# Performance work log

Hardware: AMD Instinct MI355X
Metric: run time of the kernel (lower is better)

The kernel has to match this reference:

```python
import jax, jax.numpy as jnp
import numpy as np
import math

DIM, DIM_QK, DIM_V = 1024, 128, 1024
NUM_BUCKETS, MAX_DISTANCE = 32, 128


def silu(x):
    return x * jax.nn.sigmoid(x)


def laplacian_attn_fn(x):
    mu = math.sqrt(0.5)
    std = math.sqrt(0.25 * math.pi)
    return (1.0 + jax.lax.erf((x - mu) / (std * math.sqrt(2.0)))) * 0.5


def rel_pos_bias(seq_len, table, scale):
    # causal T5 bucketing: n = q_pos - k_pos, clamped at 0
    q_pos = jnp.arange(seq_len)
    k_pos = jnp.arange(seq_len)
    rel_pos = k_pos[None, :] - q_pos[:, None]  # [i, j]
    n = jnp.maximum(-rel_pos, 0)
    max_exact = NUM_BUCKETS // 2
    is_small = n < max_exact
    n_safe = jnp.maximum(n, 1).astype(jnp.float32)
    val_if_large = max_exact + (
        jnp.log(n_safe / max_exact) / math.log(MAX_DISTANCE / max_exact)
        * (NUM_BUCKETS - max_exact)
    ).astype(jnp.int32)
    val_if_large = jnp.minimum(val_if_large, NUM_BUCKETS - 1)
    bucket = jnp.where(is_small, n, val_if_large)
    return table[bucket] * scale  # [i, j]


def setup_inputs() -> dict:
    key = jax.random.key(0)
    ks = jax.random.split(key, 8)
    B, S = 4, 2048
    lin_std_qk = 1.0 / math.sqrt(DIM)
    return {
        "x": jax.random.normal(ks[0], (B, S, DIM), dtype=jnp.float32),
        "wqk": jax.random.uniform(ks[1], (DIM, DIM_QK), minval=-lin_std_qk, maxval=lin_std_qk, dtype=jnp.float32),
        "bqk": jnp.zeros((DIM_QK,), dtype=jnp.float32),
        "gamma": 1.0 + 0.02 * jax.random.normal(ks[2], (2, DIM_QK), dtype=jnp.float32),
        "beta": jnp.zeros((2, DIM_QK), dtype=jnp.float32),
        "wv": jax.random.uniform(ks[3], (DIM, DIM_V), minval=-lin_std_qk, maxval=lin_std_qk, dtype=jnp.float32),
        "bv": jnp.zeros((DIM_V,), dtype=jnp.float32),
        "rel_bias": jax.random.normal(ks[4], (NUM_BUCKETS,), dtype=jnp.float32),
    }


def reference(x, wqk, bqk, gamma, beta, wv, bv, rel_bias):
    B, S, _ = x.shape
    qk = silu(x @ wqk + bqk)                       # [B, S, dqk]
    q = qk * gamma[0] + beta[0]
    k = qk * gamma[1] + beta[1]
    v = silu(x @ wv + bv)                          # [B, S, dv]
    scale = 1.0 / S                                # laplacian_attn_fn scaling
    sim = jnp.einsum('bid,bjd->bij', q, k) * scale
    sim = sim + rel_pos_bias(S, rel_bias, DIM_QK ** 0.5)[None, :, :]
    attn = laplacian_attn_fn(sim)
    causal_mask = jnp.triu(jnp.ones((S, S), dtype=bool), k=1)
    attn = jnp.where(causal_mask[None, :, :], 0.0, attn)
    return jnp.einsum('bij,bjd->bid', attn, v)
```

## Files before the change

### kernel.cpp

```cpp
#include <hip/hip_runtime.h>
#include <stdint.h>


#define B_   4
#define S_   2048
#define DIM_ 1024
#define DQK  128
#define DV   1024
#define NQV  1152

typedef __attribute__((ext_vector_type(8))) short short8;
typedef __attribute__((ext_vector_type(4))) float f32x4;

__device__ __forceinline__ uint16_t f32_to_bf16(float f) {
  uint32_t u = __float_as_uint(f);
  u += 0x7FFFu + ((u >> 16) & 1u);
  return (uint16_t)(u >> 16);
}

__device__ __forceinline__ uint32_t pack_bf16(float a, float b) {
  return (uint32_t)f32_to_bf16(a) | ((uint32_t)f32_to_bf16(b) << 16);
}

__device__ __forceinline__ float silu_f(float x) {
  return x * __builtin_amdgcn_rcpf(1.0f + __expf(-x));
}

__device__ __forceinline__ float laplacian_attn(float x) {
  float z  = (x - 0.70710678118654752f) * 0.79788456080286536f;
  float az = fabsf(z);
  float t  = __builtin_amdgcn_rcpf(fmaf(0.3275911f, az, 1.0f));
  float w  = fmaf(1.061405429f, t, -1.453152027f);
  w = fmaf(w, t, 1.421413741f);
  w = fmaf(w, t, -0.284496736f);
  w = fmaf(w, t, 0.254829592f);
  float P  = w * t;
  float E  = __expf(-z * z);
  float ea = fmaf(-P, E, 1.0f);
  float er = copysignf(ea, z);
  return fmaf(0.5f, er, 0.5f);
}

__device__ __forceinline__ void gload16(const uint16_t* g, uint16_t* l) {
  __builtin_amdgcn_global_load_lds(
      (const __attribute__((address_space(1))) void*)g,
      (__attribute__((address_space(3))) void*)l, 16, 0, 0);
}

template <int MT, int NT, int DEPTH>
__device__ __forceinline__ void wave_gemm_t(
    const uint16_t* __restrict__ A, int KBa, int rbA,
    const uint16_t* __restrict__ Bt, int KBb, int rbB,
    int nkb, f32x4 acc[MT][NT])
{
  const int lane = threadIdx.x & 63;

  const uint16_t* pa[MT];
  const uint16_t* pb[NT];
  #pragma unroll
  for (int mt = 0; mt < MT; mt++)
    pa[mt] = A + (size_t)(rbA + mt) * KBa * 512 + lane * 8;
  #pragma unroll
  for (int nt = 0; nt < NT; nt++)
    pb[nt] = Bt + (size_t)(rbB + nt) * KBb * 512 + lane * 8;

  #pragma unroll
  for (int mt = 0; mt < MT; mt++)
    #pragma unroll
    for (int nt = 0; nt < NT; nt++) {
      f32x4 z = {0.0f, 0.0f, 0.0f, 0.0f};
      acc[mt][nt] = z;
    }

  short8 fa0[MT], fb0[NT], fa1[MT], fb1[NT];

  auto loads = [&](short8 fa[MT], short8 fb[NT], int kb) {
    #pragma unroll
    for (int mt = 0; mt < MT; mt++)
      fa[mt] = *(const short8*)(pa[mt] + (size_t)kb * 512);
    #pragma unroll
    for (int nt = 0; nt < NT; nt++)
      fb[nt] = *(const short8*)(pb[nt] + (size_t)kb * 512);
  };
  auto mfmas = [&](short8 fa[MT], short8 fb[NT]) {
    #pragma unroll
    for (int mt = 0; mt < MT; mt++)
      #pragma unroll
      for (int nt = 0; nt < NT; nt++)
        acc[mt][nt] = __builtin_amdgcn_mfma_f32_16x16x32_bf16(
            fa[mt], fb[nt], acc[mt][nt], 0, 0, 0);
  };

  if constexpr (DEPTH == 2) {
    loads(fa0, fb0, 0);
    loads(fa1, fb1, 1);
    for (int kb = 2; kb < nkb; kb += 2) {
      mfmas(fa0, fb0);
      loads(fa0, fb0, kb);
      mfmas(fa1, fb1);
      loads(fa1, fb1, kb + 1);
    }
    mfmas(fa0, fb0);
    mfmas(fa1, fb1);
  } else {
    short8 fa2[MT], fb2[NT], fa3[MT], fb3[NT];
    loads(fa0, fb0, 0);
    loads(fa1, fb1, 1);
    loads(fa2, fb2, 2);
    loads(fa3, fb3, 3);
    for (int kb = 4; kb < nkb; kb += 4) {
      mfmas(fa0, fb0);
      loads(fa0, fb0, kb);
      mfmas(fa1, fb1);
      loads(fa1, fb1, kb + 1);
      mfmas(fa2, fb2);
      loads(fa2, fb2, kb + 2);
      mfmas(fa3, fb3);
      loads(fa3, fb3, kb + 3);
    }
    mfmas(fa0, fb0);
    mfmas(fa1, fb1);
    mfmas(fa2, fb2);
    mfmas(fa3, fb3);
  }
}

__global__ __launch_bounds__(256) void k_prep(
    const float* __restrict__ x, const float* __restrict__ wqk,
    const float* __restrict__ wv, const float* __restrict__ rel,
    uint16_t* __restrict__ xb, uint16_t* __restrict__ wT,
    float* __restrict__ bias_n)
{
  int blk = blockIdx.x;
  if (blk < 4096) {
    int t = blk * 256 + threadIdx.x;
    int i16 = t & 15, oct = (t >> 4) & 3, kb = (t >> 6) & 31, ib = t >> 11;
    const float* src = x + (size_t)(ib * 16 + i16) * DIM_ + kb * 32 + oct * 8;
    float4 a = *(const float4*)src;
    float4 b = *(const float4*)(src + 4);
    short8 o;
    o[0] = f32_to_bf16(a.x); o[1] = f32_to_bf16(a.y);
    o[2] = f32_to_bf16(a.z); o[3] = f32_to_bf16(a.w);
    o[4] = f32_to_bf16(b.x); o[5] = f32_to_bf16(b.y);
    o[6] = f32_to_bf16(b.z); o[7] = f32_to_bf16(b.w);
    *(short8*)(xb + (size_t)t * 8) = o;
  } else if (blk < 4672) {
    int t = (blk - 4096) * 256 + threadIdx.x;
    int n16 = t & 15, oct = (t >> 4) & 3, kb = (t >> 6) & 31, nb = t >> 11;
    int n = nb * 16 + n16;
    int k0 = kb * 32 + oct * 8;
    short8 o;
    if (n < DQK) {
      #pragma unroll
      for (int j = 0; j < 8; j++)
        o[j] = f32_to_bf16(wqk[(size_t)(k0 + j) * DQK + n]);
    } else {
      int nn = n - DQK;
      #pragma unroll
      for (int j = 0; j < 8; j++)
        o[j] = f32_to_bf16(wv[(size_t)(k0 + j) * DV + nn]);
    }
    *(short8*)(wT + (size_t)t * 8) = o;
  } else {
    for (int n = threadIdx.x; n < S_; n += 256) {
      int bucket;
      if (n < 16) {
        bucket = n;
      } else {
        float tt = logf((float)n * 0.0625f) / 2.0794415416798357f * 16.0f;
        int vl = 16 + (int)tt;
        bucket = vl < 31 ? vl : 31;
      }
      bias_n[n] = rel[bucket] * 11.313708498984761f;
    }
  }
}


__global__ __launch_bounds__(256, 4) void k_gemm_qkv(
    const uint16_t* __restrict__ xb, const uint16_t* __restrict__ wT,
    const float* __restrict__ bqk, const float* __restrict__ gamma,
    const float* __restrict__ beta, const float* __restrict__ bv,
    uint16_t* __restrict__ qb, uint16_t* __restrict__ kb,
    uint16_t* __restrict__ vT)
{
  int L = blockIdx.x;
  int c = L & 7;
  int idx = L >> 3;
  int by = c + 8 * (idx / 9);
  int bx = idx % 9;
  int lane = threadIdx.x & 63;
  int wave = threadIdx.x >> 6;
  int lane16 = lane & 15;
  int quad = lane >> 4;
  int wrow = (wave >> 1) * 64;
  int wcol = (wave & 1) * 64;

  __shared__ uint16_t sA[8 * 2 * 512];
  __shared__ uint16_t sB[8 * 2 * 512];

  const uint16_t *Ab, *Bb;
  if (bx == 0) { Ab = wT;                              Bb = xb + (size_t)by * 8 * 32 * 512; }
  else         { Ab = xb + (size_t)by * 8 * 32 * 512;  Bb = wT + (size_t)bx * 8 * 32 * 512; }

  const uint16_t* gp = (wave >> 1) ? Bb : Ab;
  uint16_t*       sp = (wave >> 1) ? sB : sA;
  int rb0 = (wave & 1) * 4;

  f32x4 acc[4][4];
  #pragma unroll
  for (int mt = 0; mt < 4; mt++)
    #pragma unroll
    for (int nt = 0; nt < 4; nt++) {
      f32x4 z = {0.0f, 0.0f, 0.0f, 0.0f};
      acc[mt][nt] = z;
    }

  for (int kbi = 0; kbi < 32; kbi += 2) {
    #pragma unroll
    for (int uu = 0; uu < 8; uu++) {
      int rbu = rb0 + (uu >> 1), kk = uu & 1;
      gload16(gp + ((size_t)rbu * 32 + kbi + kk) * 512 + lane * 8,
              sp + (rbu * 2 + kk) * 512);
    }
    __syncthreads();
    #pragma unroll
    for (int kk = 0; kk < 2; kk++) {
      short8 fa[4], fb[4];
      #pragma unroll
      for (int mt = 0; mt < 4; mt++)
        fa[mt] = *(const short8*)(sA + (((wave >> 1) * 4 + mt) * 2 + kk) * 512 + lane * 8);
      #pragma unroll
      for (int nt = 0; nt < 4; nt++)
        fb[nt] = *(const short8*)(sB + (((wave & 1) * 4 + nt) * 2 + kk) * 512 + lane * 8);
      #pragma unroll
      for (int mt = 0; mt < 4; mt++)
        #pragma unroll
        for (int nt = 0; nt < 4; nt++)
          acc[mt][nt] = __builtin_amdgcn_mfma_f32_16x16x32_bf16(
              fa[mt], fb[nt], acc[mt][nt], 0, 0, 0);
    }
    __syncthreads();
  }

  if (bx == 0) {
    int ibase = by * 128 + (wave & 1) * 64;
    int cbase = (wave >> 1) * 64;
    #pragma unroll
    for (int mt = 0; mt < 4; mt++) {
      int c0 = cbase + mt * 16 + quad * 4;
      float4 bb = *(const float4*)(bqk + c0);
      float4 g0 = *(const float4*)(gamma + c0);
      float4 g1 = *(const float4*)(gamma + DQK + c0);
      float4 e0 = *(const float4*)(beta + c0);
      float4 e1 = *(const float4*)(beta + DQK + c0);
      size_t coff = (size_t)(c0 >> 5) * 512 + ((c0 >> 3) & 3) * 128 + (c0 & 7);
      #pragma unroll
      for (int nt = 0; nt < 4; nt++) {
        int i = ibase + nt * 16 + lane16;
        float s0 = silu_f(acc[mt][nt][0] + bb.x);
        float s1 = silu_f(acc[mt][nt][1] + bb.y);
        float s2 = silu_f(acc[mt][nt][2] + bb.z);
        float s3 = silu_f(acc[mt][nt][3] + bb.w);
        uint2 pq, pk;
        pq.x = pack_bf16(fmaf(s0, g0.x, e0.x), fmaf(s1, g0.y, e0.y));
        pq.y = pack_bf16(fmaf(s2, g0.z, e0.z), fmaf(s3, g0.w, e0.w));
        pk.x = pack_bf16(fmaf(s0, g1.x, e1.x), fmaf(s1, g1.y, e1.y));
        pk.y = pack_bf16(fmaf(s2, g1.z, e1.z), fmaf(s3, g1.w, e1.w));
        size_t off = (size_t)(i >> 4) * 4 * 512 + (size_t)(i & 15) * 8 + coff;
        *(uint2*)(qb + off) = pq;
        *(uint2*)(kb + off) = pk;
      }
    }
  } else {
    int b = by >> 4;
    uint16_t* vt = vT + (size_t)b * DV * S_;
    #pragma unroll
    for (int nt = 0; nt < 4; nt++) {
      int n = (bx - 1) * 128 + wcol + nt * 16 + lane16;
      float bb = bv[n];
      #pragma unroll
      for (int mt = 0; mt < 4; mt++) {
        int j0l = (by & 15) * 128 + wrow + mt * 16 + quad * 4;
        uint16_t v0 = f32_to_bf16(silu_f(acc[mt][nt][0] + bb));
        uint16_t v1 = f32_to_bf16(silu_f(acc[mt][nt][1] + bb));
        uint16_t v2 = f32_to_bf16(silu_f(acc[mt][nt][2] + bb));
        uint16_t v3 = f32_to_bf16(silu_f(acc[mt][nt][3] + bb));
        size_t off = (size_t)((n >> 4) * 64 + (j0l >> 5)) * 512 +
                     ((j0l >> 3) & 3) * 128 + (n & 15) * 8 + (j0l & 7);
        uint2 pk;
        pk.x = (uint32_t)v0 | ((uint32_t)v1 << 16);
        pk.y = (uint32_t)v2 | ((uint32_t)v3 << 16);
        *(uint2*)(vt + off) = pk;
      }
    }
  }
}

__global__ __launch_bounds__(128, 6) void k_gemm_sim(
    const uint16_t* __restrict__ qb, const uint16_t* __restrict__ kb,
    const float* __restrict__ bias_n, uint16_t* __restrict__ attn)
{
  int b = blockIdx.x;
  int bt = blockIdx.y;
  int it = (int)((sqrtf(8.0f * (float)b + 1.0f) - 1.0f) * 0.5f);
  while ((it + 1) * (it + 2) / 2 <= b) ++it;
  while (it * (it + 1) / 2 > b) --it;
  int jt = b - it * (it + 1) / 2;

  int lane = threadIdx.x & 63;
  int wave = threadIdx.x >> 6;
  int lane16 = lane & 15;
  int quad = lane >> 4;

  f32x4 acc[4][2];
  wave_gemm_t<4,2,4>(kb, 4, bt * 128 + jt * 4,
                     qb, 4, bt * 128 + it * 4 + wave * 2,
                     4, acc);

  uint16_t* ab = attn + (size_t)bt * S_ * S_;
  int ibase = it * 64 + wave * 32;
  int jbase = jt * 64;
  #pragma unroll
  for (int nt = 0; nt < 2; nt++) {
    int i = ibase + nt * 16 + lane16;
    size_t irow = (size_t)(i >> 4) * 64 * 512 + (size_t)(i & 15) * 8;
    #pragma unroll
    for (int mt = 0; mt < 4; mt++) {
      int j0 = jbase + mt * 16 + quad * 4;
      float v[4];
      #pragma unroll
      for (int r = 0; r < 4; r++) {
        int j = j0 + r;
        float aval = 0.0f;
        if (j <= i) {
          float sim = acc[mt][nt][r] * (1.0f / 2048.0f) + bias_n[i - j];
          aval = laplacian_attn(sim);
        }
        v[r] = aval;
      }
      uint2 pk;
      pk.x = pack_bf16(v[0], v[1]);
      pk.y = pack_bf16(v[2], v[3]);
      size_t off = irow + (size_t)(j0 >> 5) * 512 + ((j0 >> 3) & 3) * 128 +
                   (j0 & 7);
      *(uint2*)(ab + off) = pk;
    }
  }
}

__global__ __launch_bounds__(256, 4) void k_gemm_out(
    const uint16_t* __restrict__ attn, const uint16_t* __restrict__ vT,
    float* __restrict__ out)
{
  int L = blockIdx.x;
  int c = L & 7, m = L >> 3;
  int bt = c >> 1;
  int nx = (c & 1) * 4 + (m & 3);
  int it = 15 - (m >> 2);
  int nkb = 4 * it + 4;
  int lane = threadIdx.x & 63;
  int wave = threadIdx.x >> 6;
  int lane16 = lane & 15;
  int quad = lane >> 4;
  int wrow = (wave >> 1) * 64;
  int wcol = (wave & 1) * 64;

  __shared__ uint16_t sA[8 * 2 * 512];
  __shared__ uint16_t sB[8 * 2 * 512];

  const uint16_t* Ab = vT + (size_t)bt * DV * S_ + (size_t)nx * 8 * 64 * 512;
  const uint16_t* Bb = attn + (size_t)bt * S_ * S_ + (size_t)it * 8 * 64 * 512;

  const uint16_t* gp = (wave >> 1) ? Bb : Ab;
  uint16_t*       sp = (wave >> 1) ? sB : sA;
  int rb0 = (wave & 1) * 4;

  f32x4 acc[4][4];
  #pragma unroll
  for (int mt = 0; mt < 4; mt++)
    #pragma unroll
    for (int nt = 0; nt < 4; nt++) {
      f32x4 z = {0.0f, 0.0f, 0.0f, 0.0f};
      acc[mt][nt] = z;
    }

  for (int kbi = 0; kbi < nkb; kbi += 2) {
    #pragma unroll
    for (int uu = 0; uu < 8; uu++) {
      int rbu = rb0 + (uu >> 1), kk = uu & 1;
      gload16(gp + ((size_t)rbu * 64 + kbi + kk) * 512 + lane * 8,
              sp + (rbu * 2 + kk) * 512);
    }
    __syncthreads();
    #pragma unroll
    for (int kk = 0; kk < 2; kk++) {
      short8 fa[4], fb[4];
      #pragma unroll
      for (int mt = 0; mt < 4; mt++)
        fa[mt] = *(const short8*)(sA + (((wave & 1) * 4 + mt) * 2 + kk) * 512 + lane * 8);
      #pragma unroll
      for (int nt = 0; nt < 4; nt++)
        fb[nt] = *(const short8*)(sB + (((wave >> 1) * 4 + nt) * 2 + kk) * 512 + lane * 8);
      #pragma unroll
      for (int mt = 0; mt < 4; mt++)
        #pragma unroll
        for (int nt = 0; nt < 4; nt++)
          acc[mt][nt] = __builtin_amdgcn_mfma_f32_16x16x32_bf16(
              fa[mt], fb[nt], acc[mt][nt], 0, 0, 0);
    }
    __syncthreads();
  }

  float* ob = out + ((size_t)bt * S_ + it * 128 + wrow) * DV + nx * 128 + wcol;
  #pragma unroll
  for (int nt = 0; nt < 4; nt++) {
    int i = nt * 16 + lane16;
    #pragma unroll
    for (int mt = 0; mt < 4; mt++) {
      int n = mt * 16 + quad * 4;
      *(float4*)(ob + (size_t)i * DV + n) = *(float4*)&acc[mt][nt];
    }
  }
}


extern "C" void kernel_launch(void* const* d_in, const int* in_sizes, int n_in,
                              void* d_out, int out_size, void* d_ws, size_t ws_size,
                              hipStream_t stream)
{
  const float* x     = (const float*)d_in[0];
  const float* wqk   = (const float*)d_in[1];
  const float* bqk   = (const float*)d_in[2];
  const float* gamma = (const float*)d_in[3];
  const float* beta  = (const float*)d_in[4];
  const float* wv    = (const float*)d_in[5];
  const float* bv    = (const float*)d_in[6];
  const float* rel   = (const float*)d_in[7];
  float* out = (float*)d_out;

  char* ws = (char*)d_ws;
  size_t off = 0;
  uint16_t* xb     = (uint16_t*)(ws + off); off += (size_t)B_ * S_ * DIM_ * 2;
  uint16_t* wT     = (uint16_t*)(ws + off); off += (size_t)NQV * DIM_ * 2;
  uint16_t* qb     = (uint16_t*)(ws + off); off += (size_t)B_ * S_ * DQK * 2;
  uint16_t* kb     = (uint16_t*)(ws + off); off += (size_t)B_ * S_ * DQK * 2;
  uint16_t* vT     = (uint16_t*)(ws + off); off += (size_t)B_ * DV * S_ * 2;
  uint16_t* attn   = (uint16_t*)(ws + off); off += (size_t)B_ * S_ * S_ * 2;
  float*    bias_n = (float*)(ws + off);    off += (size_t)S_ * 4;

  k_prep<<<dim3(4673), dim3(256), 0, stream>>>(x, wqk, wv, rel, xb, wT, bias_n);

  k_gemm_qkv<<<dim3(576), dim3(256), 0, stream>>>(
      xb, wT, bqk, gamma, beta, bv, qb, kb, vT);
  k_gemm_sim<<<dim3(528, B_), dim3(128), 0, stream>>>(
      qb, kb, bias_n, attn);
  k_gemm_out<<<dim3(512), dim3(256), 0, stream>>>(
      attn, vT, out);
}
```

Before: 173.0 us.

## Halve GEMM tile sizes in qkv and out kernels to double block count

Both the QKV projection GEMM and the output GEMM now use 128x64 or 64x128 tiles instead of 128x128. This doubles the grid (576→1152 and 512→1024 blocks) so the 256 CUs get better load balance and occupancy, especially for the causal, uneven-length output GEMM. The cooperative load loop is rewritten so each wave issues 6 loads over the unequal A/B panels. The trade-off is lower arithmetic intensity per block and more redundant global loads of the shared panel.

```diff
diff --git a/kernel.cpp b/kernel.cpp
--- a/kernel.cpp
+++ b/kernel.cpp
@@ -193,58 +193,57 @@
   int wave = threadIdx.x >> 6;
   int lane16 = lane & 15;
   int quad = lane >> 4;
-  int wrow = (wave >> 1) * 64;
-  int wcol = (wave & 1) * 64;
 
   __shared__ uint16_t sA[8 * 2 * 512];
   __shared__ uint16_t sB[8 * 2 * 512];
 
-  const uint16_t *Ab, *Bb;
-  if (bx == 0) { Ab = wT;                              Bb = xb + (size_t)by * 8 * 32 * 512; }
-  else         { Ab = xb + (size_t)by * 8 * 32 * 512;  Bb = wT + (size_t)bx * 8 * 32 * 512; }
-
-  const uint16_t* gp = (wave >> 1) ? Bb : Ab;
-  uint16_t*       sp = (wave >> 1) ? sB : sA;
-  int rb0 = (wave & 1) * 4;
-
-  f32x4 acc[4][4];
-  #pragma unroll
-  for (int mt = 0; mt < 4; mt++)
-    #pragma unroll
-    for (int nt = 0; nt < 4; nt++) {
-      f32x4 z = {0.0f, 0.0f, 0.0f, 0.0f};
-      acc[mt][nt] = z;
-    }
-
-  for (int kbi = 0; kbi < 32; kbi += 2) {
-    #pragma unroll
-    for (int uu = 0; uu < 8; uu++) {
-      int rbu = rb0 + (uu >> 1), kk = uu & 1;
-      gload16(gp + ((size_t)rbu * 32 + kbi + kk) * 512 + lane * 8,
-              sp + (rbu * 2 + kk) * 512);
-    }
-    __syncthreads();
-    #pragma unroll
-    for (int kk = 0; kk < 2; kk++) {
-      short8 fa[4], fb[4];
-      #pragma unroll
-      for (int mt = 0; mt < 4; mt++)
-        fa[mt] = *(const short8*)(sA + (((wave >> 1) * 4 + mt) * 2 + kk) * 512 + lane * 8);
-      #pragma unroll
-      for (int nt = 0; nt < 4; nt++)
-        fb[nt] = *(const short8*)(sB + (((wave & 1) * 4 + nt) * 2 + kk) * 512 + lane * 8);
-      #pragma unroll
-      for (int mt = 0; mt < 4; mt++)
-        #pragma unroll
-        for (int nt = 0; nt < 4; nt++)
-          acc[mt][nt] = __builtin_amdgcn_mfma_f32_16x16x32_bf16(
-              fa[mt], fb[nt], acc[mt][nt], 0, 0, 0);
-    }
-    __syncthreads();
-  }
+  const uint16_t* xpan = xb + (size_t)by * 4 * 32 * 512;
 
   if (bx == 0) {
-    int ibase = by * 128 + (wave & 1) * 64;
+    f32x4 acc[4][2];
+    #pragma unroll
+    for (int mt = 0; mt < 4; mt++)
+      #pragma unroll
+      for (int nt = 0; nt < 2; nt++) {
+        f32x4 z = {0.0f, 0.0f, 0.0f, 0.0f};
+        acc[mt][nt] = z;
+      }
+
+    for (int kbi = 0; kbi < 32; kbi += 2) {
+      #pragma unroll
+      for (int s = 0; s < 6; s++) {
+        int u = wave * 6 + s;
+        if (u < 16) {
+          int rb = u >> 1, kk = u & 1;
+          gload16(wT + ((size_t)rb * 32 + kbi + kk) * 512 + lane * 8,
+                  sA + (rb * 2 + kk) * 512);
+        } else {
+          int u2 = u - 16, rb = u2 >> 1, kk = u2 & 1;
+          gload16(xpan + ((size_t)rb * 32 + kbi + kk) * 512 + lane * 8,
+                  sB + (rb * 2 + kk) * 512);
+        }
+      }
+      __syncthreads();
+      #pragma unroll
+      for (int kk = 0; kk < 2; kk++) {
+        short8 fa[4], fb[2];
+        #pragma unroll
+        for (int mt = 0; mt < 4; mt++)
+          fa[mt] = *(const short8*)(sA + (((wave >> 1) * 4 + mt) * 2 + kk) * 512 + lane * 8);
+        #pragma unroll
+        for (int nt = 0; nt < 2; nt++)
+          fb[nt] = *(const short8*)(sB + (((wave & 1) * 2 + nt) * 2 + kk) * 512 + lane * 8);
+        #pragma unroll
+        for (int mt = 0; mt < 4; mt++)
+          #pragma unroll
+          for (int nt = 0; nt < 2; nt++)
+            acc[mt][nt] = __builtin_amdgcn_mfma_f32_16x16x32_bf16(
+                fa[mt], fb[nt], acc[mt][nt], 0, 0, 0);
+      }
+      __syncthreads();
+    }
+
+    int ibase = by * 64 + (wave & 1) * 32;
     int cbase = (wave >> 1) * 64;
     #pragma unroll
     for (int mt = 0; mt < 4; mt++) {
@@ -256,7 +255,7 @@
       float4 e1 = *(const float4*)(beta + DQK + c0);
       size_t coff = (size_t)(c0 >> 5) * 512 + ((c0 >> 3) & 3) * 128 + (c0 & 7);
       #pragma unroll
-      for (int nt = 0; nt < 4; nt++) {
+      for (int nt = 0; nt < 2; nt++) {
         int i = ibase + nt * 16 + lane16;
         float s0 = silu_f(acc[mt][nt][0] + bb.x);
         float s1 = silu_f(acc[mt][nt][1] + bb.y);
@@ -273,15 +272,59 @@
       }
     }
   } else {
-    int b = by >> 4;
+    const uint16_t* wpan = wT + (size_t)bx * 8 * 32 * 512;
+    f32x4 acc[2][4];
+    #pragma unroll
+    for (int mt = 0; mt < 2; mt++)
+      #pragma unroll
+      for (int nt = 0; nt < 4; nt++) {
+        f32x4 z = {0.0f, 0.0f, 0.0f, 0.0f};
+        acc[mt][nt] = z;
+      }
+
+    for (int kbi = 0; kbi < 32; kbi += 2) {
+      #pragma unroll
+      for (int s = 0; s < 6; s++) {
+        int u = wave * 6 + s;
+        if (u < 8) {
+          int rb = u >> 1, kk = u & 1;
+          gload16(xpan + ((size_t)rb * 32 + kbi + kk) * 512 + lane * 8,
+                  sA + (rb * 2 + kk) * 512);
+        } else {
+          int u2 = u - 8, rb = u2 >> 1, kk = u2 & 1;
+          gload16(wpan + ((size_t)rb * 32 + kbi + kk) * 512 + lane * 8,
+                  sB + (rb * 2 + kk) * 512);
+        }
+      }
+      __syncthreads();
+      #pragma unroll
+      for (int kk = 0; kk < 2; kk++) {
+        short8 fa[2], fb[4];
+        #pragma unroll
+        for (int mt = 0; mt < 2; mt++)
+          fa[mt] = *(const short8*)(sA + (((wave >> 1) * 2 + mt) * 2 + kk) * 512 + lane * 8);
+        #pragma unroll
+        for (int nt = 0; nt < 4; nt++)
+          fb[nt] = *(const short8*)(sB + (((wave & 1) * 4 + nt) * 2 + kk) * 512 + lane * 8);
+        #pragma unroll
+        for (int mt = 0; mt < 2; mt++)
+          #pragma unroll
+          for (int nt = 0; nt < 4; nt++)
+            acc[mt][nt] = __builtin_amdgcn_mfma_f32_16x16x32_bf16(
+                fa[mt], fb[nt], acc[mt][nt], 0, 0, 0);
+      }
+      __syncthreads();
+    }
+
+    int b = by >> 5;
     uint16_t* vt = vT + (size_t)b * DV * S_;
     #pragma unroll
     for (int nt = 0; nt < 4; nt++) {
-      int n = (bx - 1) * 128 + wcol + nt * 16 + lane16;
+      int n = (bx - 1) * 128 + (wave & 1) * 64 + nt * 16 + lane16;
       float bb = bv[n];
       #pragma unroll
-      for (int mt = 0; mt < 4; mt++) {
-        int j0l = (by & 15) * 128 + wrow + mt * 16 + quad * 4;
+      for (int mt = 0; mt < 2; mt++) {
+        int j0l = (by & 31) * 64 + (wave >> 1) * 32 + mt * 16 + quad * 4;
         uint16_t v0 = f32_to_bf16(silu_f(acc[mt][nt][0] + bb));
         uint16_t v1 = f32_to_bf16(silu_f(acc[mt][nt][1] + bb));
         uint16_t v2 = f32_to_bf16(silu_f(acc[mt][nt][2] + bb));
@@ -356,29 +399,23 @@
   int L = blockIdx.x;
   int c = L & 7, m = L >> 3;
   int bt = c >> 1;
-  int nx = (c & 1) * 4 + (m & 3);
-  int it = 15 - (m >> 2);
+  int nx = (c & 1) * 8 + (m & 7);
+  int it = 15 - (m >> 3);
   int nkb = 4 * it + 4;
   int lane = threadIdx.x & 63;
   int wave = threadIdx.x >> 6;
   int lane16 = lane & 15;
   int quad = lane >> 4;
-  int wrow = (wave >> 1) * 64;
-  int wcol = (wave & 1) * 64;
-
-  __shared__ uint16_t sA[8 * 2 * 512];
+
+  __shared__ uint16_t sA[4 * 2 * 512];
   __shared__ uint16_t sB[8 * 2 * 512];
 
-  const uint16_t* Ab = vT + (size_t)bt * DV * S_ + (size_t)nx * 8 * 64 * 512;
+  const uint16_t* Ab = vT + (size_t)bt * DV * S_ + (size_t)nx * 4 * 64 * 512;
   const uint16_t* Bb = attn + (size_t)bt * S_ * S_ + (size_t)it * 8 * 64 * 512;
 
-  const uint16_t* gp = (wave >> 1) ? Bb : Ab;
-  uint16_t*       sp = (wave >> 1) ? sB : sA;
-  int rb0 = (wave & 1) * 4;
-
-  f32x4 acc[4][4];
+  f32x4 acc[2][4];
   #pragma unroll
-  for (int mt = 0; mt < 4; mt++)
+  for (int mt = 0; mt < 2; mt++)
     #pragma unroll
     for (int nt = 0; nt < 4; nt++) {
       f32x4 z = {0.0f, 0.0f, 0.0f, 0.0f};
@@ -387,23 +424,30 @@
 
   for (int kbi = 0; kbi < nkb; kbi += 2) {
     #pragma unroll
-    for (int uu = 0; uu < 8; uu++) {
-      int rbu = rb0 + (uu >> 1), kk = uu & 1;
-      gload16(gp + ((size_t)rbu * 64 + kbi + kk) * 512 + lane * 8,
-              sp + (rbu * 2 + kk) * 512);
+    for (int s = 0; s < 6; s++) {
+      int u = wave * 6 + s;
+      if (u < 8) {
+        int rb = u >> 1, kk = u & 1;
+        gload16(Ab + ((size_t)rb * 64 + kbi + kk) * 512 + lane * 8,
+                sA + (rb * 2 + kk) * 512);
+      } else {
+        int u2 = u - 8, rb = u2 >> 1, kk = u2 & 1;
+        gload16(Bb + ((size_t)rb * 64 + kbi + kk) * 512 + lane * 8,
+                sB + (rb * 2 + kk) * 512);
+      }
     }
     __syncthreads();
     #pragma unroll
     for (int kk = 0; kk < 2; kk++) {
-      short8 fa[4], fb[4];
-      #pragma unroll
-      for (int mt = 0; mt < 4; mt++)
-        fa[mt] = *(const short8*)(sA + (((wave & 1) * 4 + mt) * 2 + kk) * 512 + lane * 8);
+      short8 fa[2], fb[4];
+      #pragma unroll
+      for (int mt = 0; mt < 2; mt++)
+        fa[mt] = *(const short8*)(sA + (((wave & 1) * 2 + mt) * 2 + kk) * 512 + lane * 8);
       #pragma unroll
       for (int nt = 0; nt < 4; nt++)
         fb[nt] = *(const short8*)(sB + (((wave >> 1) * 4 + nt) * 2 + kk) * 512 + lane * 8);
       #pragma unroll
-      for (int mt = 0; mt < 4; mt++)
+      for (int mt = 0; mt < 2; mt++)
         #pragma unroll
         for (int nt = 0; nt < 4; nt++)
           acc[mt][nt] = __builtin_amdgcn_mfma_f32_16x16x32_bf16(
@@ -412,12 +456,13 @@
     __syncthreads();
   }
 
-  float* ob = out + ((size_t)bt * S_ + it * 128 + wrow) * DV + nx * 128 + wcol;
+  float* ob = out + ((size_t)bt * S_ + it * 128 + (wave >> 1) * 64) * DV +
+              nx * 64 + (wave & 1) * 32;
   #pragma unroll
   for (int nt = 0; nt < 4; nt++) {
     int i = nt * 16 + lane16;
     #pragma unroll
-    for (int mt = 0; mt < 4; mt++) {
+    for (int mt = 0; mt < 2; mt++) {
       int n = mt * 16 + quad * 4;
       *(float4*)(ob + (size_t)i * DV + n) = *(float4*)&acc[mt][nt];
     }
@@ -451,10 +496,10 @@
 
   k_prep<<<dim3(4673), dim3(256), 0, stream>>>(x, wqk, wv, rel, xb, wT, bias_n);
 
-  k_gemm_qkv<<<dim3(576), dim3(256), 0, stream>>>(
+  k_gemm_qkv<<<dim3(1152), dim3(256), 0, stream>>>(
       xb, wT, bqk, gamma, beta, bv, qb, kb, vT);
   k_gemm_sim<<<dim3(528, B_), dim3(128), 0, stream>>>(
       qb, kb, bias_n, attn);
-  k_gemm_out<<<dim3(512), dim3(256), 0, stream>>>(
+  k_gemm_out<<<dim3(1024), dim3(256), 0, stream>>>(
       attn, vT, out);
 }
```

Measured after the change: 173.4 us. No clear change (+0.2%).

## Double-buffer LDS staging in QKV and output GEMMs, retune launch bounds

Applied to the files above, without the earlier changes.

The QKV-projection and attention-output GEMMs now use two LDS buffers, one k-block each. The next k-block is prefetched into the other buffer while MFMAs run on the current one, with a single barrier per iteration instead of two. This aims to overlap global-to-LDS loads with matrix math. In exchange, occupancy hints drop (4→3 for the GEMMs, 6→4 for the sim kernel), and a wave_gemm_t template parameter in the sim kernel changes from 4 to 2, likely its stage or unroll depth. Each iteration now does half as much work per sync, so there are more loop iterations.

```diff
diff --git a/kernel.cpp b/kernel.cpp
--- a/kernel.cpp
+++ b/kernel.cpp
@@ -177,7 +177,7 @@
 }
 
 
-__global__ __launch_bounds__(256, 4) void k_gemm_qkv(
+__global__ __launch_bounds__(256, 3) void k_gemm_qkv(
     const uint16_t* __restrict__ xb, const uint16_t* __restrict__ wT,
     const float* __restrict__ bqk, const float* __restrict__ gamma,
     const float* __restrict__ beta, const float* __restrict__ bv,
@@ -196,16 +196,25 @@
   int wrow = (wave >> 1) * 64;
   int wcol = (wave & 1) * 64;
 
-  __shared__ uint16_t sA[8 * 2 * 512];
-  __shared__ uint16_t sB[8 * 2 * 512];
+  __shared__ uint16_t sA[2][8 * 512];
+  __shared__ uint16_t sB[2][8 * 512];
 
   const uint16_t *Ab, *Bb;
   if (bx == 0) { Ab = wT;                              Bb = xb + (size_t)by * 8 * 32 * 512; }
   else         { Ab = xb + (size_t)by * 8 * 32 * 512;  Bb = wT + (size_t)bx * 8 * 32 * 512; }
 
   const uint16_t* gp = (wave >> 1) ? Bb : Ab;
-  uint16_t*       sp = (wave >> 1) ? sB : sA;
   int rb0 = (wave & 1) * 4;
+
+  auto stage = [&](int b, int kbi) {
+    uint16_t* sp = (wave >> 1) ? sB[b] : sA[b];
+    #pragma unroll
+    for (int r = 0; r < 4; r++) {
+      int rbu = rb0 + r;
+      gload16(gp + ((size_t)rbu * 32 + kbi) * 512 + lane * 8,
+              sp + rbu * 512);
+    }
+  };
 
   f32x4 acc[4][4];
   #pragma unroll
@@ -216,31 +225,25 @@
       acc[mt][nt] = z;
     }
 
-  for (int kbi = 0; kbi < 32; kbi += 2) {
-    #pragma unroll
-    for (int uu = 0; uu < 8; uu++) {
-      int rbu = rb0 + (uu >> 1), kk = uu & 1;
-      gload16(gp + ((size_t)rbu * 32 + kbi + kk) * 512 + lane * 8,
-              sp + (rbu * 2 + kk) * 512);
-    }
+  stage(0, 0);
+  int cur = 0;
+  for (int kbi = 0; kbi < 32; ++kbi) {
     __syncthreads();
-    #pragma unroll
-    for (int kk = 0; kk < 2; kk++) {
-      short8 fa[4], fb[4];
-      #pragma unroll
-      for (int mt = 0; mt < 4; mt++)
-        fa[mt] = *(const short8*)(sA + (((wave >> 1) * 4 + mt) * 2 + kk) * 512 + lane * 8);
+    if (kbi + 1 < 32) stage(cur ^ 1, kbi + 1);
+    short8 fa[4], fb[4];
+    #pragma unroll
+    for (int mt = 0; mt < 4; mt++)
+      fa[mt] = *(const short8*)(sA[cur] + ((wave >> 1) * 4 + mt) * 512 + lane * 8);
+    #pragma unroll
+    for (int nt = 0; nt < 4; nt++)
+      fb[nt] = *(const short8*)(sB[cur] + ((wave & 1) * 4 + nt) * 512 + lane * 8);
+    #pragma unroll
+    for (int mt = 0; mt < 4; mt++)
       #pragma unroll
       for (int nt = 0; nt < 4; nt++)
-        fb[nt] = *(const short8*)(sB + (((wave & 1) * 4 + nt) * 2 + kk) * 512 + lane * 8);
-      #pragma unroll
-      for (int mt = 0; mt < 4; mt++)
-        #pragma unroll
-        for (int nt = 0; nt < 4; nt++)
-          acc[mt][nt] = __builtin_amdgcn_mfma_f32_16x16x32_bf16(
-              fa[mt], fb[nt], acc[mt][nt], 0, 0, 0);
-    }
-    __syncthreads();
+        acc[mt][nt] = __builtin_amdgcn_mfma_f32_16x16x32_bf16(
+            fa[mt], fb[nt], acc[mt][nt], 0, 0, 0);
+    cur ^= 1;
   }
 
   if (bx == 0) {
@@ -297,7 +300,7 @@
   }
 }
 
-__global__ __launch_bounds__(128, 6) void k_gemm_sim(
+__global__ __launch_bounds__(128, 4) void k_gemm_sim(
     const uint16_t* __restrict__ qb, const uint16_t* __restrict__ kb,
     const float* __restrict__ bias_n, uint16_t* __restrict__ attn)
 {
@@ -314,7 +317,7 @@
   int quad = lane >> 4;
 
   f32x4 acc[4][2];
-  wave_gemm_t<4,2,4>(kb, 4, bt * 128 + jt * 4,
+  wave_gemm_t<4,2,2>(kb, 4, bt * 128 + jt * 4,
                      qb, 4, bt * 128 + it * 4 + wave * 2,
                      4, acc);
 
@@ -349,7 +352,7 @@
   }
 }
 
-__global__ __launch_bounds__(256, 4) void k_gemm_out(
+__global__ __launch_bounds__(256, 3) void k_gemm_out(
     const uint16_t* __restrict__ attn, const uint16_t* __restrict__ vT,
     float* __restrict__ out)
 {
@@ -366,15 +369,24 @@
   int wrow = (wave >> 1) * 64;
   int wcol = (wave & 1) * 64;
 
-  __shared__ uint16_t sA[8 * 2 * 512];
-  __shared__ uint16_t sB[8 * 2 * 512];
+  __shared__ uint16_t sA[2][8 * 512];
+  __shared__ uint16_t sB[2][8 * 512];
 
   const uint16_t* Ab = vT + (size_t)bt * DV * S_ + (size_t)nx * 8 * 64 * 512;
   const uint16_t* Bb = attn + (size_t)bt * S_ * S_ + (size_t)it * 8 * 64 * 512;
 
   const uint16_t* gp = (wave >> 1) ? Bb : Ab;
-  uint16_t*       sp = (wave >> 1) ? sB : sA;
   int rb0 = (wave & 1) * 4;
+
+  auto stage = [&](int b, int kbi) {
+    uint16_t* sp = (wave >> 1) ? sB[b] : sA[b];
+    #pragma unroll
+    for (int r = 0; r < 4; r++) {
+      int rbu = rb0 + r;
+      gload16(gp + ((size_t)rbu * 64 + kbi) * 512 + lane * 8,
+              sp + rbu * 512);
+    }
+  };
 
   f32x4 acc[4][4];
   #pragma unroll
@@ -385,31 +397,25 @@
       acc[mt][nt] = z;
     }
 
-  for (int kbi = 0; kbi < nkb; kbi += 2) {
-    #pragma unroll
-    for (int uu = 0; uu < 8; uu++) {
-      int rbu = rb0 + (uu >> 1), kk = uu & 1;
-      gload16(gp + ((size_t)rbu * 64 + kbi + kk) * 512 + lane * 8,
-              sp + (rbu * 2 + kk) * 512);
-    }
+  stage(0, 0);
+  int cur = 0;
+  for (int kbi = 0; kbi < nkb; ++kbi) {
     __syncthreads();
-    #pragma unroll
-    for (int kk = 0; kk < 2; kk++) {
-      short8 fa[4], fb[4];
-      #pragma unroll
-      for (int mt = 0; mt < 4; mt++)
-        fa[mt] = *(const short8*)(sA + (((wave & 1) * 4 + mt) * 2 + kk) * 512 + lane * 8);
+    if (kbi + 1 < nkb) stage(cur ^ 1, kbi + 1);
+    short8 fa[4], fb[4];
+    #pragma unroll
+    for (int mt = 0; mt < 4; mt++)
+      fa[mt] = *(const short8*)(sA[cur] + ((wave & 1) * 4 + mt) * 512 + lane * 8);
+    #pragma unroll
+    for (int nt = 0; nt < 4; nt++)
+      fb[nt] = *(const short8*)(sB[cur] + ((wave >> 1) * 4 + nt) * 512 + lane * 8);
+    #pragma unroll
+    for (int mt = 0; mt < 4; mt++)
       #pragma unroll
       for (int nt = 0; nt < 4; nt++)
-        fb[nt] = *(const short8*)(sB + (((wave >> 1) * 4 + nt) * 2 + kk) * 512 + lane * 8);
-      #pragma unroll
-      for (int mt = 0; mt < 4; mt++)
-        #pragma unroll
-        for (int nt = 0; nt < 4; nt++)
-          acc[mt][nt] = __builtin_amdgcn_mfma_f32_16x16x32_bf16(
-              fa[mt], fb[nt], acc[mt][nt], 0, 0, 0);
-    }
-    __syncthreads();
+        acc[mt][nt] = __builtin_amdgcn_mfma_f32_16x16x32_bf16(
+            fa[mt], fb[nt], acc[mt][nt], 0, 0, 0);
+    cur ^= 1;
   }
 
   float* ob = out + ((size_t)bt * S_ + it * 128 + wrow) * DV + nx * 128 + wcol;
```

Result: faster. 169.0 us (-2.3%).
